# Kernel optimization log

Hardware: AMD Instinct MI355X
Metric: run time of the kernel (lower is better)

## Reference

```python
import jax, jax.numpy as jnp
import numpy as np

B, S, E, H, V, C = 64, 512, 256, 128, 50000, 2


def setup_inputs() -> dict:
    key = jax.random.key(0)
    ks = jax.random.split(key, 12)
    sentences = jax.random.randint(ks[0], (B, S), 0, V, dtype=jnp.int32)
    # sparse binary adjacency (dependency-tree-like), float for bmm
    adj = (jax.random.uniform(ks[1], (B, S, S)) < 0.05).astype(jnp.float32)
    emb_table = jax.random.normal(ks[2], (V, E), dtype=jnp.float32) * 0.02
    W1 = jax.random.normal(ks[3], (H, E), dtype=jnp.float32) * 0.05
    b1 = jnp.zeros((H,), jnp.float32)
    W2 = jax.random.normal(ks[4], (H, H), dtype=jnp.float32) * 0.05
    b2 = jnp.zeros((H,), jnp.float32)
    W3 = jax.random.normal(ks[5], (H, H), dtype=jnp.float32) * 0.05
    b3 = jnp.zeros((H,), jnp.float32)
    Wp = jax.random.normal(ks[6], (C, H), dtype=jnp.float32) * 0.05
    bp = jnp.zeros((C,), jnp.float32)
    return {"sentences": sentences, "adj": adj, "emb_table": emb_table,
            "W1": W1, "b1": b1, "W2": W2, "b2": b2, "W3": W3, "b3": b3,
            "Wp": Wp, "bp": bp}


def reference(sentences, adj, emb_table, W1, b1, W2, b2, W3, b3, Wp, bp):
    # embedding lookup (dropout is eval-mode identity)
    h = emb_table[sentences]  # [B, S, E]
    # degree normalization term (self-loop adds +1)
    deg = jnp.sum(adj, axis=-1, keepdims=True) + 1.0  # [B, S, 1]
    for W, b in ((W1, b1), (W2, b2), (W3, b3)):
        agg = jnp.einsum('bst,btd->bsd', adj, h)  # bmm(adj, h)
        # layer(agg) + layer(h) == (agg + h) @ W^T + 2b  (shared weights)
        h = ((agg + h) @ W.T + 2.0 * b) / deg
        h = jax.nn.relu(h)
    # AdaptiveMaxPool1d(1) over sequence dim
    pooled = jnp.max(h, axis=1)  # [B, H]
    logits = pooled @ Wp.T + bp  # [B, C]
    return logits
```

## Files before the change

kernel.cpp:

```cpp
#include <hip/hip_runtime.h>

typedef unsigned short ushort_t;
typedef unsigned long long ull_t;

#define B_ 64
#define S_ 512
#define E_ 256
#define H_ 128
#define M_ (B_ * S_)
#define CAP_ 128

__global__ void k_adjidx(const float* __restrict__ adj,
                         ushort_t* __restrict__ idxl,
                         int* __restrict__ nnz,
                         float* __restrict__ invdeg) {
    int row  = blockIdx.x * 4 + (threadIdx.x >> 6);
    int lane = threadIdx.x & 63;
    const float4* arow = (const float4*)(adj + (size_t)row * S_);
    ushort_t* dst = idxl + (size_t)row * CAP_;
    int total = 0;
    #pragma unroll
    for (int c = 0; c < 2; ++c) {
        float4 v = arow[c * 64 + lane];
        float f[4] = {v.x, v.y, v.z, v.w};
        #pragma unroll
        for (int j = 0; j < 4; ++j) {
            unsigned long long m = __ballot(f[j] != 0.0f);
            if (f[j] != 0.0f) {
                int pos = total + __popcll(m & ((1ull << lane) - 1ull));
                if (pos < CAP_) dst[pos] = (ushort_t)(c * 256 + lane * 4 + j);
            }
            total += __popcll(m);
        }
    }
    if (lane == 0) {
        nnz[row] = total < CAP_ ? total : CAP_;
        invdeg[row] = 1.0f / (float)(total + 1);
    }
}

template <int K, bool GATHER, bool POOL>
__global__ __launch_bounds__(512, 4)
void k_layer(const float* __restrict__ X, const int* __restrict__ sent,
             const float* __restrict__ emb, const float* __restrict__ W,
             const ushort_t* __restrict__ idxl, const int* __restrict__ nnz,
             const float* __restrict__ invdeg, const float* __restrict__ bias,
             float* __restrict__ out) {
    __shared__ __align__(16) float Ys[S_ * 20];
    __shared__ __align__(16) float Xs[2][8 * S_];
    __shared__ __align__(16) float Wsh[2][8 * 16];

    const int tid = threadIdx.x;
    const int bid = blockIdx.x;
    const int b  = (bid & 7) + 8 * (bid >> 6);
    const int cg = (bid >> 3) & 7;
    const int colBase = cg * 16;
    const int rowBase = b * S_;

    const float* xp;
    if (GATHER) xp = emb + (size_t)sent[rowBase + tid] * K;
    else        xp = X + (size_t)(rowBase + tid) * K;

    const int wcol = tid & 15;
    const int kq4  = (tid >> 4) * 4;
    const float* wp = W + (size_t)(colBase + wcol) * K + kq4;

    const int rg4 = tid & ~3;
    const int c0  = (tid & 3) * 4;

    float acc[4][4] = {};
    float4 g0, g1;
    float4 wv = {0.f, 0.f, 0.f, 0.f};

    constexpr int NC = K / 8;

    g0 = *(const float4*)(xp);
    g1 = *(const float4*)(xp + 4);
    if (tid < 32) wv = *(const float4*)(wp);
    Xs[0][0 * 512 + tid] = g0.x;
    Xs[0][1 * 512 + tid] = g0.y;
    Xs[0][2 * 512 + tid] = g0.z;
    Xs[0][3 * 512 + tid] = g0.w;
    Xs[0][4 * 512 + tid] = g1.x;
    Xs[0][5 * 512 + tid] = g1.y;
    Xs[0][6 * 512 + tid] = g1.z;
    Xs[0][7 * 512 + tid] = g1.w;
    if (tid < 32) {
        Wsh[0][(kq4 + 0) * 16 + wcol] = wv.x;
        Wsh[0][(kq4 + 1) * 16 + wcol] = wv.y;
        Wsh[0][(kq4 + 2) * 16 + wcol] = wv.z;
        Wsh[0][(kq4 + 3) * 16 + wcol] = wv.w;
    }
    __syncthreads();

    #pragma unroll 1
    for (int c = 0; c < NC; ++c) {
        const int cur = c & 1;
        if (c + 1 < NC) {
            g0 = *(const float4*)(xp + (c + 1) * 8);
            g1 = *(const float4*)(xp + (c + 1) * 8 + 4);
            if (tid < 32) wv = *(const float4*)(wp + (c + 1) * 8);
        }
        #pragma unroll
        for (int k = 0; k < 8; ++k) {
            const float4 xa = *(const float4*)&Xs[cur][k * 512 + rg4];
            const float4 wa = *(const float4*)&Wsh[cur][k * 16 + c0];
            const float xv[4] = {xa.x, xa.y, xa.z, xa.w};
            const float wf[4] = {wa.x, wa.y, wa.z, wa.w};
            #pragma unroll
            for (int i = 0; i < 4; ++i)
                #pragma unroll
                for (int j = 0; j < 4; ++j)
                    acc[i][j] += xv[i] * wf[j];
        }
        if (c + 1 < NC) {
            const int nb = cur ^ 1;
            Xs[nb][0 * 512 + tid] = g0.x;
            Xs[nb][1 * 512 + tid] = g0.y;
            Xs[nb][2 * 512 + tid] = g0.z;
            Xs[nb][3 * 512 + tid] = g0.w;
            Xs[nb][4 * 512 + tid] = g1.x;
            Xs[nb][5 * 512 + tid] = g1.y;
            Xs[nb][6 * 512 + tid] = g1.z;
            Xs[nb][7 * 512 + tid] = g1.w;
            if (tid < 32) {
                Wsh[nb][(kq4 + 0) * 16 + wcol] = wv.x;
                Wsh[nb][(kq4 + 1) * 16 + wcol] = wv.y;
                Wsh[nb][(kq4 + 2) * 16 + wcol] = wv.z;
                Wsh[nb][(kq4 + 3) * 16 + wcol] = wv.w;
            }
        }
        __syncthreads();
    }

    #pragma unroll
    for (int i = 0; i < 4; ++i)
        *(float4*)&Ys[(rg4 + i) * 20 + c0] =
            make_float4(acc[i][0], acc[i][1], acc[i][2], acc[i][3]);
    __syncthreads();

    const int rsub = tid >> 2;
    const int cc   = tid & 3;
    const float4* Ys4 = (const float4*)Ys;
    const float4 bv = *(const float4*)(bias + colBase + cc * 4);
    float4 pmax = {0.f, 0.f, 0.f, 0.f};

    #pragma unroll 1
    for (int p = 0; p < 4; ++p) {
        const int r = p * 128 + rsub;
        const int grow = rowBase + r;
        const int n = nnz[grow];
        const float inv = invdeg[grow];
        const ushort_t* il = idxl + (size_t)grow * CAP_;
        float4 a = Ys4[r * 5 + cc];
        float4 a2 = {0.f, 0.f, 0.f, 0.f};
        int i = 0;
        #pragma unroll 1
        for (; i + 8 <= n; i += 8) {
            const ull_t pka = *(const ull_t*)(il + i);
            const ull_t pkb = *(const ull_t*)(il + i + 4);
            const int t0 = (int)(pka & 0xffffu);
            const int t1 = (int)((pka >> 16) & 0xffffu);
            const int t2 = (int)((pka >> 32) & 0xffffu);
            const int t3 = (int)(pka >> 48);
            const int t4 = (int)(pkb & 0xffffu);
            const int t5 = (int)((pkb >> 16) & 0xffffu);
            const int t6 = (int)((pkb >> 32) & 0xffffu);
            const int t7 = (int)(pkb >> 48);
            const float4 v0 = Ys4[t0 * 5 + cc];
            const float4 v1 = Ys4[t1 * 5 + cc];
            const float4 v2 = Ys4[t2 * 5 + cc];
            const float4 v3 = Ys4[t3 * 5 + cc];
            const float4 v4 = Ys4[t4 * 5 + cc];
            const float4 v5 = Ys4[t5 * 5 + cc];
            const float4 v6 = Ys4[t6 * 5 + cc];
            const float4 v7 = Ys4[t7 * 5 + cc];
            a.x += v0.x + v1.x;  a.y += v0.y + v1.y;
            a.z += v0.z + v1.z;  a.w += v0.w + v1.w;
            a2.x += v2.x + v3.x; a2.y += v2.y + v3.y;
            a2.z += v2.z + v3.z; a2.w += v2.w + v3.w;
            a.x += v4.x + v5.x;  a.y += v4.y + v5.y;
            a.z += v4.z + v5.z;  a.w += v4.w + v5.w;
            a2.x += v6.x + v7.x; a2.y += v6.y + v7.y;
            a2.z += v6.z + v7.z; a2.w += v6.w + v7.w;
        }
        for (; i + 4 <= n; i += 4) {
            const ull_t pka = *(const ull_t*)(il + i);
            const int t0 = (int)(pka & 0xffffu);
            const int t1 = (int)((pka >> 16) & 0xffffu);
            const int t2 = (int)((pka >> 32) & 0xffffu);
            const int t3 = (int)(pka >> 48);
            const float4 v0 = Ys4[t0 * 5 + cc];
            const float4 v1 = Ys4[t1 * 5 + cc];
            const float4 v2 = Ys4[t2 * 5 + cc];
            const float4 v3 = Ys4[t3 * 5 + cc];
            a.x += v0.x + v1.x;  a.y += v0.y + v1.y;
            a.z += v0.z + v1.z;  a.w += v0.w + v1.w;
            a2.x += v2.x + v3.x; a2.y += v2.y + v3.y;
            a2.z += v2.z + v3.z; a2.w += v2.w + v3.w;
        }
        for (; i < n; ++i) {
            const int t = il[i];
            const float4 v = Ys4[t * 5 + cc];
            a.x += v.x; a.y += v.y; a.z += v.z; a.w += v.w;
        }
        a.x += a2.x; a.y += a2.y; a.z += a2.z; a.w += a2.w;
        float4 o;
        o.x = fmaxf((a.x + 2.0f * bv.x) * inv, 0.0f);
        o.y = fmaxf((a.y + 2.0f * bv.y) * inv, 0.0f);
        o.z = fmaxf((a.z + 2.0f * bv.z) * inv, 0.0f);
        o.w = fmaxf((a.w + 2.0f * bv.w) * inv, 0.0f);
        if (!POOL) {
            *(float4*)(out + (size_t)grow * H_ + colBase + cc * 4) = o;
        } else {
            pmax.x = fmaxf(pmax.x, o.x); pmax.y = fmaxf(pmax.y, o.y);
            pmax.z = fmaxf(pmax.z, o.z); pmax.w = fmaxf(pmax.w, o.w);
        }
    }

    if (POOL) {
        float4* smax = (float4*)Xs;
        smax[tid] = pmax;
        __syncthreads();
        if (tid < 64) {
            const int gg = tid >> 2, c2 = tid & 3;
            float4 m = smax[gg * 4 + c2];
            #pragma unroll
            for (int j = 1; j < 8; ++j) {
                const float4 v = smax[(gg + 16 * j) * 4 + c2];
                m.x = fmaxf(m.x, v.x); m.y = fmaxf(m.y, v.y);
                m.z = fmaxf(m.z, v.z); m.w = fmaxf(m.w, v.w);
            }
            smax[512 + gg * 4 + c2] = m;
        }
        __syncthreads();
        if (tid < 4) {
            float4 m = smax[512 + tid];
            #pragma unroll
            for (int g = 1; g < 16; ++g) {
                const float4 v = smax[512 + g * 4 + tid];
                m.x = fmaxf(m.x, v.x); m.y = fmaxf(m.y, v.y);
                m.z = fmaxf(m.z, v.z); m.w = fmaxf(m.w, v.w);
            }
            *(float4*)(out + (size_t)b * H_ + colBase + tid * 4) = m;
        }
    }
}

__global__ void k_final(const float* __restrict__ pooled,
                        const float* __restrict__ Wp,
                        const float* __restrict__ bp,
                        float* __restrict__ out) {
    int b = blockIdx.x, j = threadIdx.x;
    float m = pooled[(size_t)b * H_ + j];
    float t0 = m * Wp[j];
    float t1 = m * Wp[H_ + j];
    #pragma unroll
    for (int off = 32; off > 0; off >>= 1) {
        t0 += __shfl_down(t0, off);
        t1 += __shfl_down(t1, off);
    }
    __shared__ float red[2][2];
    int wave = j >> 6, lane = j & 63;
    if (lane == 0) { red[0][wave] = t0; red[1][wave] = t1; }
    __syncthreads();
    if (j == 0) out[b * 2 + 0] = red[0][0] + red[0][1] + bp[0];
    if (j == 1) out[b * 2 + 1] = red[1][0] + red[1][1] + bp[1];
}

extern "C" void kernel_launch(void* const* d_in, const int* in_sizes, int n_in,
                              void* d_out, int out_size, void* d_ws, size_t ws_size,
                              hipStream_t stream) {
    const int*   sent = (const int*)d_in[0];
    const float* adj  = (const float*)d_in[1];
    const float* emb  = (const float*)d_in[2];
    const float* W1   = (const float*)d_in[3];
    const float* b1   = (const float*)d_in[4];
    const float* W2   = (const float*)d_in[5];
    const float* b2   = (const float*)d_in[6];
    const float* W3   = (const float*)d_in[7];
    const float* b3   = (const float*)d_in[8];
    const float* Wp   = (const float*)d_in[9];
    const float* bp   = (const float*)d_in[10];
    float* out = (float*)d_out;

    char* ws = (char*)d_ws;
    float*    h1     = (float*)ws;
    float*    h2     = (float*)(ws + ((size_t)16 << 20));
    char*     base   = ws + ((size_t)32 << 20);
    float*    invdeg = (float*)base;
    int*      nnz    = (int*)(base + (size_t)M_ * 4);
    ushort_t* idxl   = (ushort_t*)(base + (size_t)M_ * 8);
    float*    pooled = (float*)(base + (size_t)M_ * 8 + (size_t)M_ * CAP_ * 2);

    k_adjidx<<<M_ / 4, 256, 0, stream>>>(adj, idxl, nnz, invdeg);

    k_layer<E_, true,  false><<<512, 512, 0, stream>>>(nullptr, sent, emb, W1, idxl, nnz, invdeg, b1, h1);
    k_layer<H_, false, false><<<512, 512, 0, stream>>>(h1, nullptr, nullptr, W2, idxl, nnz, invdeg, b2, h2);
    k_layer<H_, false, true ><<<512, 512, 0, stream>>>(h2, nullptr, nullptr, W3, idxl, nnz, invdeg, b3, pooled);

    k_final<<<B_, H_, 0, stream>>>(pooled, Wp, bp, out);
}
```

Before: 279.1 us.

## Stage neighbor index lists in swizzled LDS and prefetch per-row metadata early

Halves the per-row neighbor index capacity and loads each block's index lists with coalesced float4 reads into shared memory (XOR-swizzled, in two halves of 256 rows), replacing scattered global ushort loads inside the gather loop. nnz and invdeg are fetched at kernel start so their latency overlaps the GEMM phase, and the next 8 indices are software-prefetched from LDS. The pooled max reduction moves to the Ys buffer. Lowering the capacity to 64 risks truncating rows with more than 64 neighbors, although the 5% density gives about 26 on average.

```diff
diff --git a/kernel.cpp b/kernel.cpp
--- a/kernel.cpp
+++ b/kernel.cpp
@@ -8,7 +8,7 @@
 #define E_ 256
 #define H_ 128
 #define M_ (B_ * S_)
-#define CAP_ 128
+#define CAP_ 64
 
 __global__ void k_adjidx(const float* __restrict__ adj,
                          ushort_t* __restrict__ idxl,
@@ -57,6 +57,18 @@
     const int colBase = cg * 16;
     const int rowBase = b * S_;
 
+    const int rsub = tid >> 2;
+    const int cc   = tid & 3;
+    int   nn0, nn1, nn2, nn3;
+    float iv0, iv1, iv2, iv3;
+    {
+        const int g0r = rowBase + rsub;
+        nn0 = nnz[g0r];       iv0 = invdeg[g0r];
+        nn1 = nnz[g0r + 128]; iv1 = invdeg[g0r + 128];
+        nn2 = nnz[g0r + 256]; iv2 = invdeg[g0r + 256];
+        nn3 = nnz[g0r + 384]; iv3 = invdeg[g0r + 384];
+    }
+
     const float* xp;
     if (GATHER) xp = emb + (size_t)sent[rowBase + tid] * K;
     else        xp = X + (size_t)(rowBase + tid) * K;
@@ -133,40 +145,65 @@
         __syncthreads();
     }
 
+    const float4* ilg = (const float4*)(idxl + (size_t)rowBase * CAP_);
+    float4 sA0 = ilg[tid * 4 + 0];
+    float4 sA1 = ilg[tid * 4 + 1];
+    float4 sA2 = ilg[tid * 4 + 2];
+    float4 sA3 = ilg[tid * 4 + 3];
+
     #pragma unroll
     for (int i = 0; i < 4; ++i)
         *(float4*)&Ys[(rg4 + i) * 20 + c0] =
             make_float4(acc[i][0], acc[i][1], acc[i][2], acc[i][3]);
     __syncthreads();
 
-    const int rsub = tid >> 2;
-    const int cc   = tid & 3;
-    const float4* Ys4 = (const float4*)Ys;
+    float4* xs4 = (float4*)Xs;
+    {
+        const int r = tid >> 1, jb = (tid & 1) * 4, s = r & 7;
+        xs4[r * 8 + ((jb + 0) ^ s)] = sA0;
+        xs4[r * 8 + ((jb + 1) ^ s)] = sA1;
+        xs4[r * 8 + ((jb + 2) ^ s)] = sA2;
+        xs4[r * 8 + ((jb + 3) ^ s)] = sA3;
+    }
+    float4 sB0 = ilg[2048 + tid * 4 + 0];
+    float4 sB1 = ilg[2048 + tid * 4 + 1];
+    float4 sB2 = ilg[2048 + tid * 4 + 2];
+    float4 sB3 = ilg[2048 + tid * 4 + 3];
+    __syncthreads();
+
+    const float4*   Ys4   = (const float4*)Ys;
+    const ull_t*    xsu   = (const ull_t*)Xs;
+    const ushort_t* xsu16 = (const ushort_t*)Xs;
     const float4 bv = *(const float4*)(bias + colBase + cc * 4);
     float4 pmax = {0.f, 0.f, 0.f, 0.f};
 
-    #pragma unroll 1
-    for (int p = 0; p < 4; ++p) {
-        const int r = p * 128 + rsub;
-        const int grow = rowBase + r;
-        const int n = nnz[grow];
-        const float inv = invdeg[grow];
-        const ushort_t* il = idxl + (size_t)grow * CAP_;
+    auto gather_pass = [&](int P, int n, float inv) {
+        const int r  = P * 128 + rsub;
+        const int lr = r & 255;
+        const int s  = lr & 7;
+        const int rb16 = lr * 16;
         float4 a = Ys4[r * 5 + cc];
         float4 a2 = {0.f, 0.f, 0.f, 0.f};
+        ull_t pka = xsu[rb16 + (s << 1)];
+        ull_t pkb = xsu[rb16 + (s << 1) + 1];
         int i = 0;
         #pragma unroll 1
         for (; i + 8 <= n; i += 8) {
-            const ull_t pka = *(const ull_t*)(il + i);
-            const ull_t pkb = *(const ull_t*)(il + i + 4);
-            const int t0 = (int)(pka & 0xffffu);
-            const int t1 = (int)((pka >> 16) & 0xffffu);
-            const int t2 = (int)((pka >> 32) & 0xffffu);
-            const int t3 = (int)(pka >> 48);
-            const int t4 = (int)(pkb & 0xffffu);
-            const int t5 = (int)((pkb >> 16) & 0xffffu);
-            const int t6 = (int)((pkb >> 32) & 0xffffu);
-            const int t7 = (int)(pkb >> 48);
+            const ull_t pa = pka, pb = pkb;
+            const int i2 = i + 8;
+            if (i2 + 8 <= n) {
+                const int j = ((i2 >> 3) ^ s) << 1;
+                pka = xsu[rb16 + j];
+                pkb = xsu[rb16 + j + 1];
+            }
+            const int t0 = (int)(pa & 0xffffu);
+            const int t1 = (int)((pa >> 16) & 0xffffu);
+            const int t2 = (int)((pa >> 32) & 0xffffu);
+            const int t3 = (int)(pa >> 48);
+            const int t4 = (int)(pb & 0xffffu);
+            const int t5 = (int)((pb >> 16) & 0xffffu);
+            const int t6 = (int)((pb >> 32) & 0xffffu);
+            const int t7 = (int)(pb >> 48);
             const float4 v0 = Ys4[t0 * 5 + cc];
             const float4 v1 = Ys4[t1 * 5 + cc];
             const float4 v2 = Ys4[t2 * 5 + cc];
@@ -184,12 +221,12 @@
             a2.x += v6.x + v7.x; a2.y += v6.y + v7.y;
             a2.z += v6.z + v7.z; a2.w += v6.w + v7.w;
         }
-        for (; i + 4 <= n; i += 4) {
-            const ull_t pka = *(const ull_t*)(il + i);
-            const int t0 = (int)(pka & 0xffffu);
-            const int t1 = (int)((pka >> 16) & 0xffffu);
-            const int t2 = (int)((pka >> 32) & 0xffffu);
-            const int t3 = (int)(pka >> 48);
+        if (i + 4 <= n) {
+            const ull_t pa = xsu[rb16 + (((i >> 3) ^ s) << 1)];
+            const int t0 = (int)(pa & 0xffffu);
+            const int t1 = (int)((pa >> 16) & 0xffffu);
+            const int t2 = (int)((pa >> 32) & 0xffffu);
+            const int t3 = (int)(pa >> 48);
             const float4 v0 = Ys4[t0 * 5 + cc];
             const float4 v1 = Ys4[t1 * 5 + cc];
             const float4 v2 = Ys4[t2 * 5 + cc];
@@ -198,9 +235,11 @@
             a.z += v0.z + v1.z;  a.w += v0.w + v1.w;
             a2.x += v2.x + v3.x; a2.y += v2.y + v3.y;
             a2.z += v2.z + v3.z; a2.w += v2.w + v3.w;
-        }
+            i += 4;
+        }
+        #pragma unroll 1
         for (; i < n; ++i) {
-            const int t = il[i];
+            const int t = xsu16[lr * 64 + (((i >> 3) ^ s) << 3) + (i & 7)];
             const float4 v = Ys4[t * 5 + cc];
             a.x += v.x; a.y += v.y; a.z += v.z; a.w += v.w;
         }
@@ -211,15 +250,32 @@
         o.z = fmaxf((a.z + 2.0f * bv.z) * inv, 0.0f);
         o.w = fmaxf((a.w + 2.0f * bv.w) * inv, 0.0f);
         if (!POOL) {
-            *(float4*)(out + (size_t)grow * H_ + colBase + cc * 4) = o;
+            *(float4*)(out + (size_t)(rowBase + r) * H_ + colBase + cc * 4) = o;
         } else {
             pmax.x = fmaxf(pmax.x, o.x); pmax.y = fmaxf(pmax.y, o.y);
             pmax.z = fmaxf(pmax.z, o.z); pmax.w = fmaxf(pmax.w, o.w);
         }
-    }
+    };
+
+    gather_pass(0, nn0, iv0);
+    gather_pass(1, nn1, iv1);
+
+    __syncthreads();
+    {
+        const int r = tid >> 1, jb = (tid & 1) * 4, s = r & 7;
+        xs4[r * 8 + ((jb + 0) ^ s)] = sB0;
+        xs4[r * 8 + ((jb + 1) ^ s)] = sB1;
+        xs4[r * 8 + ((jb + 2) ^ s)] = sB2;
+        xs4[r * 8 + ((jb + 3) ^ s)] = sB3;
+    }
+    __syncthreads();
+
+    gather_pass(2, nn2, iv2);
+    gather_pass(3, nn3, iv3);
 
     if (POOL) {
-        float4* smax = (float4*)Xs;
+        __syncthreads();
+        float4* smax = (float4*)Ys;
         smax[tid] = pmax;
         __syncthreads();
         if (tid < 64) {
```

New measurement: 280.2 us. Within noise of the previous version (+0.4%).

## Stream X rows from registers instead of LDS staging in fused layer GEMM

Applied to the files above, without the earlier changes.

The GEMM phase drops the double-buffered X tile in shared memory. Each thread now loads its four rows directly from global memory with a one-step register prefetch, while the weight slice is staged in LDS 128 K-values at a time. This removes most LDS traffic and per-chunk barriers and cuts LDS footprint, which may raise occupancy. It also halves the neighbour-list capacity to 64, prefetches packed indices in the gather loop, and hoists the nnz/invdeg loads. The trade-offs are strided, uncoalesced per-thread global loads of X rows and silent truncation of any row with more than 64 neighbours.

```diff
diff --git a/kernel.cpp b/kernel.cpp
--- a/kernel.cpp
+++ b/kernel.cpp
@@ -8,7 +8,7 @@
 #define E_ 256
 #define H_ 128
 #define M_ (B_ * S_)
-#define CAP_ 128
+#define CAP_ 64
 
 __global__ void k_adjidx(const float* __restrict__ adj,
                          ushort_t* __restrict__ idxl,
@@ -47,8 +47,7 @@
              const float* __restrict__ invdeg, const float* __restrict__ bias,
              float* __restrict__ out) {
     __shared__ __align__(16) float Ys[S_ * 20];
-    __shared__ __align__(16) float Xs[2][8 * S_];
-    __shared__ __align__(16) float Wsh[2][8 * 16];
+    __shared__ __align__(16) float Wsh[128 * 16];
 
     const int tid = threadIdx.x;
     const int bid = blockIdx.x;
@@ -57,116 +56,113 @@
     const int colBase = cg * 16;
     const int rowBase = b * S_;
 
-    const float* xp;
-    if (GATHER) xp = emb + (size_t)sent[rowBase + tid] * K;
-    else        xp = X + (size_t)(rowBase + tid) * K;
-
-    const int wcol = tid & 15;
-    const int kq4  = (tid >> 4) * 4;
-    const float* wp = W + (size_t)(colBase + wcol) * K + kq4;
-
-    const int rg4 = tid & ~3;
-    const int c0  = (tid & 3) * 4;
+    const int rg   = tid >> 2;
+    const int c4   = tid & 3;
+    const int row0 = rg * 4;
+
+    const float* xr0; const float* xr1; const float* xr2; const float* xr3;
+    if (GATHER) {
+        xr0 = emb + (size_t)sent[rowBase + row0 + 0] * K;
+        xr1 = emb + (size_t)sent[rowBase + row0 + 1] * K;
+        xr2 = emb + (size_t)sent[rowBase + row0 + 2] * K;
+        xr3 = emb + (size_t)sent[rowBase + row0 + 3] * K;
+    } else {
+        xr0 = X + (size_t)(rowBase + row0) * K;
+        xr1 = xr0 + K; xr2 = xr0 + 2 * K; xr3 = xr0 + 3 * K;
+    }
 
     float acc[4][4] = {};
-    float4 g0, g1;
-    float4 wv = {0.f, 0.f, 0.f, 0.f};
-
-    constexpr int NC = K / 8;
-
-    g0 = *(const float4*)(xp);
-    g1 = *(const float4*)(xp + 4);
-    if (tid < 32) wv = *(const float4*)(wp);
-    Xs[0][0 * 512 + tid] = g0.x;
-    Xs[0][1 * 512 + tid] = g0.y;
-    Xs[0][2 * 512 + tid] = g0.z;
-    Xs[0][3 * 512 + tid] = g0.w;
-    Xs[0][4 * 512 + tid] = g1.x;
-    Xs[0][5 * 512 + tid] = g1.y;
-    Xs[0][6 * 512 + tid] = g1.z;
-    Xs[0][7 * 512 + tid] = g1.w;
-    if (tid < 32) {
-        Wsh[0][(kq4 + 0) * 16 + wcol] = wv.x;
-        Wsh[0][(kq4 + 1) * 16 + wcol] = wv.y;
-        Wsh[0][(kq4 + 2) * 16 + wcol] = wv.z;
-        Wsh[0][(kq4 + 3) * 16 + wcol] = wv.w;
-    }
-    __syncthreads();
 
     #pragma unroll 1
-    for (int c = 0; c < NC; ++c) {
-        const int cur = c & 1;
-        if (c + 1 < NC) {
-            g0 = *(const float4*)(xp + (c + 1) * 8);
-            g1 = *(const float4*)(xp + (c + 1) * 8 + 4);
-            if (tid < 32) wv = *(const float4*)(wp + (c + 1) * 8);
-        }
-        #pragma unroll
-        for (int k = 0; k < 8; ++k) {
-            const float4 xa = *(const float4*)&Xs[cur][k * 512 + rg4];
-            const float4 wa = *(const float4*)&Wsh[cur][k * 16 + c0];
-            const float xv[4] = {xa.x, xa.y, xa.z, xa.w};
-            const float wf[4] = {wa.x, wa.y, wa.z, wa.w};
+    for (int kh = 0; kh < K; kh += 128) {
+        if (kh) __syncthreads();
+        {
+            const int c = tid & 15, kq = tid >> 4;
+            const float* wp = W + (size_t)(colBase + c) * K + kh + kq * 4;
+            const float4 wv = *(const float4*)wp;
+            Wsh[(kq * 4 + 0) * 16 + c] = wv.x;
+            Wsh[(kq * 4 + 1) * 16 + c] = wv.y;
+            Wsh[(kq * 4 + 2) * 16 + c] = wv.z;
+            Wsh[(kq * 4 + 3) * 16 + c] = wv.w;
+        }
+        __syncthreads();
+
+        float4 x0 = *(const float4*)(xr0 + kh);
+        float4 x1 = *(const float4*)(xr1 + kh);
+        float4 x2 = *(const float4*)(xr2 + kh);
+        float4 x3 = *(const float4*)(xr3 + kh);
+
+        #pragma unroll 1
+        for (int g = 0; g < 32; ++g) {
+            float4 n0, n1, n2, n3;
+            const bool more = (g + 1 < 32);
+            if (more) {
+                n0 = *(const float4*)(xr0 + kh + (g + 1) * 4);
+                n1 = *(const float4*)(xr1 + kh + (g + 1) * 4);
+                n2 = *(const float4*)(xr2 + kh + (g + 1) * 4);
+                n3 = *(const float4*)(xr3 + kh + (g + 1) * 4);
+            }
             #pragma unroll
-            for (int i = 0; i < 4; ++i)
-                #pragma unroll
-                for (int j = 0; j < 4; ++j)
-                    acc[i][j] += xv[i] * wf[j];
-        }
-        if (c + 1 < NC) {
-            const int nb = cur ^ 1;
-            Xs[nb][0 * 512 + tid] = g0.x;
-            Xs[nb][1 * 512 + tid] = g0.y;
-            Xs[nb][2 * 512 + tid] = g0.z;
-            Xs[nb][3 * 512 + tid] = g0.w;
-            Xs[nb][4 * 512 + tid] = g1.x;
-            Xs[nb][5 * 512 + tid] = g1.y;
-            Xs[nb][6 * 512 + tid] = g1.z;
-            Xs[nb][7 * 512 + tid] = g1.w;
-            if (tid < 32) {
-                Wsh[nb][(kq4 + 0) * 16 + wcol] = wv.x;
-                Wsh[nb][(kq4 + 1) * 16 + wcol] = wv.y;
-                Wsh[nb][(kq4 + 2) * 16 + wcol] = wv.z;
-                Wsh[nb][(kq4 + 3) * 16 + wcol] = wv.w;
-            }
-        }
-        __syncthreads();
-    }
+            for (int kk = 0; kk < 4; ++kk) {
+                const float4 wv = *(const float4*)&Wsh[(g * 4 + kk) * 16 + c4 * 4];
+                const float e0 = (kk == 0) ? x0.x : (kk == 1) ? x0.y : (kk == 2) ? x0.z : x0.w;
+                const float e1 = (kk == 0) ? x1.x : (kk == 1) ? x1.y : (kk == 2) ? x1.z : x1.w;
+                const float e2 = (kk == 0) ? x2.x : (kk == 1) ? x2.y : (kk == 2) ? x2.z : x2.w;
+                const float e3 = (kk == 0) ? x3.x : (kk == 1) ? x3.y : (kk == 2) ? x3.z : x3.w;
+                acc[0][0] += e0 * wv.x; acc[0][1] += e0 * wv.y;
+                acc[0][2] += e0 * wv.z; acc[0][3] += e0 * wv.w;
+                acc[1][0] += e1 * wv.x; acc[1][1] += e1 * wv.y;
+                acc[1][2] += e1 * wv.z; acc[1][3] += e1 * wv.w;
+                acc[2][0] += e2 * wv.x; acc[2][1] += e2 * wv.y;
+                acc[2][2] += e2 * wv.z; acc[2][3] += e2 * wv.w;
+                acc[3][0] += e3 * wv.x; acc[3][1] += e3 * wv.y;
+                acc[3][2] += e3 * wv.z; acc[3][3] += e3 * wv.w;
+            }
+            if (more) { x0 = n0; x1 = n1; x2 = n2; x3 = n3; }
+        }
+    }
+
+    const int rsub = rg;
+    const int cc   = c4;
+    const int g0r = rowBase + rsub;
+    const int   nn0 = nnz[g0r];        const float ivA = invdeg[g0r];
+    const int   nn1 = nnz[g0r + 128];  const float ivB = invdeg[g0r + 128];
+    const int   nn2 = nnz[g0r + 256];  const float ivC = invdeg[g0r + 256];
+    const int   nn3 = nnz[g0r + 384];  const float ivD = invdeg[g0r + 384];
 
     #pragma unroll
     for (int i = 0; i < 4; ++i)
-        *(float4*)&Ys[(rg4 + i) * 20 + c0] =
+        *(float4*)&Ys[(row0 + i) * 20 + c4 * 4] =
             make_float4(acc[i][0], acc[i][1], acc[i][2], acc[i][3]);
     __syncthreads();
 
-    const int rsub = tid >> 2;
-    const int cc   = tid & 3;
     const float4* Ys4 = (const float4*)Ys;
     const float4 bv = *(const float4*)(bias + colBase + cc * 4);
     float4 pmax = {0.f, 0.f, 0.f, 0.f};
 
-    #pragma unroll 1
-    for (int p = 0; p < 4; ++p) {
-        const int r = p * 128 + rsub;
-        const int grow = rowBase + r;
-        const int n = nnz[grow];
-        const float inv = invdeg[grow];
-        const ushort_t* il = idxl + (size_t)grow * CAP_;
+    auto gather_pass = [&](int P, int n, float inv) {
+        const int r = P * 128 + rsub;
+        const ull_t* il64 = (const ull_t*)(idxl + (size_t)(rowBase + r) * CAP_);
         float4 a = Ys4[r * 5 + cc];
         float4 a2 = {0.f, 0.f, 0.f, 0.f};
+        ull_t pka = il64[0];
+        ull_t pkb = il64[1];
         int i = 0;
         #pragma unroll 1
         for (; i + 8 <= n; i += 8) {
-            const ull_t pka = *(const ull_t*)(il + i);
-            const ull_t pkb = *(const ull_t*)(il + i + 4);
-            const int t0 = (int)(pka & 0xffffu);
-            const int t1 = (int)((pka >> 16) & 0xffffu);
-            const int t2 = (int)((pka >> 32) & 0xffffu);
-            const int t3 = (int)(pka >> 48);
-            const int t4 = (int)(pkb & 0xffffu);
-            const int t5 = (int)((pkb >> 16) & 0xffffu);
-            const int t6 = (int)((pkb >> 32) & 0xffffu);
-            const int t7 = (int)(pkb >> 48);
+            const ull_t pa = pka, pb = pkb;
+            if (i + 16 <= n) {
+                pka = il64[(i >> 2) + 2];
+                pkb = il64[(i >> 2) + 3];
+            }
+            const int t0 = (int)(pa & 0xffffu);
+            const int t1 = (int)((pa >> 16) & 0xffffu);
+            const int t2 = (int)((pa >> 32) & 0xffffu);
+            const int t3 = (int)(pa >> 48);
+            const int t4 = (int)(pb & 0xffffu);
+            const int t5 = (int)((pb >> 16) & 0xffffu);
+            const int t6 = (int)((pb >> 32) & 0xffffu);
+            const int t7 = (int)(pb >> 48);
             const float4 v0 = Ys4[t0 * 5 + cc];
             const float4 v1 = Ys4[t1 * 5 + cc];
             const float4 v2 = Ys4[t2 * 5 + cc];
@@ -184,12 +180,12 @@
             a2.x += v6.x + v7.x; a2.y += v6.y + v7.y;
             a2.z += v6.z + v7.z; a2.w += v6.w + v7.w;
         }
-        for (; i + 4 <= n; i += 4) {
-            const ull_t pka = *(const ull_t*)(il + i);
-            const int t0 = (int)(pka & 0xffffu);
-            const int t1 = (int)((pka >> 16) & 0xffffu);
-            const int t2 = (int)((pka >> 32) & 0xffffu);
-            const int t3 = (int)(pka >> 48);
+        if (i + 4 <= n) {
+            const ull_t pa = il64[i >> 2];
+            const int t0 = (int)(pa & 0xffffu);
+            const int t1 = (int)((pa >> 16) & 0xffffu);
+            const int t2 = (int)((pa >> 32) & 0xffffu);
+            const int t3 = (int)(pa >> 48);
             const float4 v0 = Ys4[t0 * 5 + cc];
             const float4 v1 = Ys4[t1 * 5 + cc];
             const float4 v2 = Ys4[t2 * 5 + cc];
@@ -198,9 +194,12 @@
             a.z += v0.z + v1.z;  a.w += v0.w + v1.w;
             a2.x += v2.x + v3.x; a2.y += v2.y + v3.y;
             a2.z += v2.z + v3.z; a2.w += v2.w + v3.w;
-        }
+            i += 4;
+        }
+        const ushort_t* il16 = (const ushort_t*)il64;
+        #pragma unroll 1
         for (; i < n; ++i) {
-            const int t = il[i];
+            const int t = il16[i];
             const float4 v = Ys4[t * 5 + cc];
             a.x += v.x; a.y += v.y; a.z += v.z; a.w += v.w;
         }
@@ -211,15 +210,21 @@
         o.z = fmaxf((a.z + 2.0f * bv.z) * inv, 0.0f);
         o.w = fmaxf((a.w + 2.0f * bv.w) * inv, 0.0f);
         if (!POOL) {
-            *(float4*)(out + (size_t)grow * H_ + colBase + cc * 4) = o;
+            *(float4*)(out + (size_t)(rowBase + r) * H_ + colBase + cc * 4) = o;
         } else {
             pmax.x = fmaxf(pmax.x, o.x); pmax.y = fmaxf(pmax.y, o.y);
             pmax.z = fmaxf(pmax.z, o.z); pmax.w = fmaxf(pmax.w, o.w);
         }
-    }
+    };
+
+    gather_pass(0, nn0, ivA);
+    gather_pass(1, nn1, ivB);
+    gather_pass(2, nn2, ivC);
+    gather_pass(3, nn3, ivD);
 
     if (POOL) {
-        float4* smax = (float4*)Xs;
+        __syncthreads();
+        float4* smax = (float4*)Ys;
         smax[tid] = pmax;
         __syncthreads();
         if (tid < 64) {
```

Result: slower. 322.6 us (+15.6%).
